# Kernel optimization log

Measured on AMD Instinct MI355X. Metric: run time of the kernel, lower is better.

Reference implementation:

```python
import jax, jax.numpy as jnp
import numpy as np
from itertools import combinations

WIRES, LAYERS, CUTOFF, OUT_WIRES, BATCH = 4, 2, 10, 3, 2048

def _annih(c):
    # annihilation operator a in the Fock basis, truncated to cutoff c
    return jnp.diag(jnp.sqrt(jnp.arange(1, c, dtype=jnp.float32)), 1).astype(jnp.complex64)

_expm = jnp.vectorize(jax.scipy.linalg.expm, signature='(n,n)->(n,n)')

def _squeeze(r, phi, a):
    # S(z) = exp((z* a^2 - z a+^2)/2), z = r e^{i phi}; r, phi have arbitrary batch shape
    z = (r * jnp.exp(1j * phi)).astype(jnp.complex64)[..., None, None]
    a2 = a @ a
    ad2 = a.conj().T @ a.conj().T
    return _expm(0.5 * (jnp.conj(z) * a2 - z * ad2))

def _disp(r, phi, a):
    # D(alpha) = exp(alpha a+ - alpha* a), alpha = r e^{i phi}
    al = (r * jnp.exp(1j * phi)).astype(jnp.complex64)[..., None, None]
    ad = a.conj().T
    return _expm(al * ad - jnp.conj(al) * a)

def _bs(theta, phi, a):
    # SF BSgate: B = exp(theta (e^{i phi} a b+ - e^{-i phi} a+ b))
    ad = a.conj().T
    G = theta * (jnp.exp(1j * phi) * jnp.kron(a, ad) - jnp.exp(-1j * phi) * jnp.kron(ad, a))
    return jax.scipy.linalg.expm(G.astype(jnp.complex64))

def _cx(s, a):
    # SF CXgate: exp(-i s x1 p2 / hbar) = exp(-(s/2) (a+a+) kron (b-b+)) with hbar=2
    ad = a.conj().T
    G = (-s / 2.0) * jnp.kron(a + ad, a - ad)
    return jax.scipy.linalg.expm(G.astype(jnp.complex64))

def _apply1(state, U, m):
    # apply single-mode gate U ([c,c] shared or [B,c,c] per-sample) to mode m
    if U.ndim == 2:
        return jnp.moveaxis(jnp.tensordot(state, U, axes=[[1 + m], [1]]), -1, 1 + m)
    st = jnp.moveaxis(state, 1 + m, -1)
    st = jnp.einsum('b...j,bij->b...i', st, U)
    return jnp.moveaxis(st, -1, 1 + m)

def _apply2(state, U4, m1, m2):
    # apply two-mode gate U4 [c,c,c,c] (out1,out2,in1,in2) to modes (m1, m2)
    st = jnp.moveaxis(state, (1 + m1, 1 + m2), (-2, -1))
    st = jnp.einsum('b...kl,ijkl->b...ij', st, U4)
    return jnp.moveaxis(st, (-2, -1), (1 + m1, 1 + m2))

def _forward(jets, s_scale, disp_mag, disp_phase, squeeze_mag, squeeze_phase, w_dense, b_dense):
    B, c = jets.shape[0], CUTOFF
    a = _annih(c)
    eta, phi, pt = jets[:, :, 0], jets[:, :, 1], jets[:, :, 2]  # each [B, WIRES]
    scale = 10.0 / (1.0 + jnp.exp(-s_scale)) + 0.01
    # vacuum |0...0> for every sample
    state = jnp.zeros((B,) + (c,) * WIRES, jnp.complex64)
    state = state.at[(slice(None),) + (0,) * WIRES].set(1.0)
    # per-sample data-encoding gates
    S_enc = _squeeze(eta, pt * phi / 2.0, a)      # [B, WIRES, c, c]
    D_enc = _disp(scale * pt, eta, a)             # [B, WIRES, c, c]
    for w in range(WIRES):
        state = _apply1(state, S_enc[:, w], w)
        state = _apply1(state, D_enc[:, w], w)
    # fixed entangling gates (shared across batch)
    CX = _cx(1.0, a).reshape(c, c, c, c)
    BS = _bs(jnp.pi / 4.0, jnp.pi / 2.0, a).reshape(c, c, c, c)
    # learned per-layer single-mode gates (shared across batch)
    S_lay = _squeeze(squeeze_mag, squeeze_phase, a)  # [LAYERS, WIRES, c, c]
    D_lay = _disp(disp_mag, disp_phase, a)
    for L in range(LAYERS):
        for (i, j) in combinations(range(WIRES), 2):
            state = _apply2(state, CX, i, j)
        for i in range(WIRES):
            state = _apply2(state, BS, i, (i + 1) % WIRES)
        for w in range(WIRES):
            state = _apply1(state, S_lay[L, w], w)
            state = _apply1(state, D_lay[L, w], w)
    probs = jnp.abs(state) ** 2
    nvec = jnp.arange(c, dtype=jnp.float32)
    photons = jnp.stack(
        [probs.sum(axis=tuple(1 + k for k in range(WIRES) if k != m)) @ nvec
         for m in range(OUT_WIRES)], axis=1)  # [B, OUT_WIRES] mean photon numbers
    return (photons @ w_dense + b_dense)[:, 0]  # [B]

def setup_inputs() -> dict:
    key = jax.random.key(0)
    ks = jax.random.split(key, 8)
    u = lambda k, sh: jax.random.uniform(k, sh, jnp.float32, -1.0, 1.0)
    return {
        'jets': 0.3 * jax.random.normal(ks[0], (BATCH, WIRES, 3), jnp.float32),
        's_scale': u(ks[1], ()),
        'disp_mag': u(ks[2], (LAYERS, WIRES)),
        'disp_phase': u(ks[3], (LAYERS, WIRES)),
        'squeeze_mag': u(ks[4], (LAYERS, WIRES)),
        'squeeze_phase': u(ks[5], (LAYERS, WIRES)),
        'w_dense': u(ks[6], (OUT_WIRES, 1)),
        'b_dense': jnp.zeros((1,), jnp.float32),
    }

def reference(jets, s_scale, disp_mag, disp_phase, squeeze_mag, squeeze_phase, w_dense, b_dense):
    return _forward(jets, s_scale, disp_mag, disp_phase, squeeze_mag, squeeze_phase, w_dense, b_dense)
```

## Files before the change

kernel.cpp:

```cpp
#include <hip/hip_runtime.h>
#include <math.h>


namespace {

constexpr int NTB = 1024;
constexpr int SMEM_STATE = 162352;
constexpr double THETA = 0.7853981633974483096;

struct cxf { float x, y; };
typedef float v2f __attribute__((ext_vector_type(2)));
typedef float v4f __attribute__((ext_vector_type(4)));

constexpr int U_OFF = 15872;

__device__ __forceinline__ cxf gen_squeeze_f(int i, int j, float zr, float zi){
  if (j == i+2){ float g = 0.5f*sqrtf((float)((i+1)*(i+2))); return {zr*g, -zi*g}; }
  if (i == j+2){ float g = 0.5f*sqrtf((float)((j+1)*(j+2))); return {-zr*g, -zi*g}; }
  return {0.f, 0.f};
}
__device__ __forceinline__ cxf gen_disp_f(int i, int j, float ar, float ai){
  if (i == j+1){ float g = sqrtf((float)i); return {ar*g, ai*g}; }
  if (j == i+1){ float g = sqrtf((float)j); return {-ar*g, ai*g}; }
  return {0.f, 0.f};
}

__device__ void expm_f32(bool act, int n, cxf* M, cxf* P, cxf* T, cxf* R, int lane){
  const int n2 = n*n;
  if (act){
    for (int e=lane; e<n2; e+=64){ M[e].x *= 0x1p-10f; M[e].y *= 0x1p-10f; }
    for (int e=lane; e<n2; e+=64){
      P[e] = M[e];
      cxf r = M[e];
      if (e % (n+1) == 0) r.x += 1.f;
      R[e] = r;
    }
  }
  __syncthreads();
  for (int t=2; t<=12; ++t){
    if (act){
      float inv = 1.f/(float)t;
      for (int e=lane; e<n2; e+=64){
        int i = e/n, j = e - i*n;
        float ax=0.f, ay=0.f;
        for (int k=0;k<n;k++){
          cxf p = P[i*n+k], m = M[k*n+j];
          ax += p.x*m.x - p.y*m.y;
          ay += p.x*m.y + p.y*m.x;
        }
        T[e] = {ax*inv, ay*inv};
      }
    }
    __syncthreads();
    { cxf* tmp = P; P = T; T = tmp; }
    if (act){ for (int e=lane; e<n2; e+=64){ R[e].x += P[e].x; R[e].y += P[e].y; } }
    __syncthreads();
  }
  for (int s=0; s<10; ++s){
    if (act){
      for (int e=lane; e<n2; e+=64){
        int i = e/n, j = e - i*n;
        float ax=0.f, ay=0.f;
        for (int k=0;k<n;k++){
          cxf p = R[i*n+k], q = R[k*n+j];
          ax += p.x*q.x - p.y*q.y;
          ay += p.x*q.y + p.y*q.x;
        }
        T[e] = {ax, ay};
      }
    }
    __syncthreads();
    { cxf* tmp = R; R = T; T = tmp; }
    __syncthreads();
  }
}

__global__ __launch_bounds__(256)
void gates_kernel(const float* __restrict__ dmag, const float* __restrict__ dphase,
                  const float* __restrict__ smag, const float* __restrict__ sphase,
                  float* __restrict__ wsf){
  __shared__ double lam[10];
  __shared__ float scr[4][4][200];
  const int tid = threadIdx.x;
  const int wv = tid >> 6, lane = tid & 63, g = blockIdx.x;
  float* ws_V  = wsf;
  float* ws_VT = wsf + 100;
  float* ws_W  = wsf + 200;
  cxf* ws_BS   = (cxf*)(wsf + 1200);
  cxf* ws_stage= (cxf*)(wsf + 6600);

  if (tid < 10){
    double lo = -6.0, hi = 6.0;
    for (int it=0; it<52; ++it){
      double mid = 0.5*(lo+hi);
      int cnt = 0;
      double pm1 = 1.0;
      double p = -mid;
      if (p == 0.0){ p = -1e-300; }
      if (p < 0.0) cnt++;
      for (int k=2; k<=10; ++k){
        double pn = -mid*p - (double)(k-1)*pm1;
        bool chg = (pn < 0.0) != (p < 0.0);
        if (pn == 0.0){ pn = (p < 0.0) ? 1e-300 : -1e-300; chg = true; }
        if (chg) cnt++;
        pm1 = p; p = pn;
      }
      if (cnt > tid) hi = mid; else lo = mid;
    }
    double x = 0.5*(lo+hi);
    double p[10];
    p[0] = 1.0; p[1] = x;
    for (int k=1;k<9;k++) p[k+1] = (x*p[k] - sqrt((double)k)*p[k-1]) * (1.0/sqrt((double)(k+1)));
    double nn=0.0; for (int k=0;k<10;k++) nn += p[k]*p[k];
    double inv = 1.0/sqrt(nn);
    lam[tid] = x;
    if (g == 0){
      for (int k=0;k<10;k++){
        float v = (float)(p[k]*inv);
        ws_V[k*10+tid]  = v;
        ws_VT[tid*10+k] = v;
      }
    }
  }
  __syncthreads();

  int t = g*4 + wv;
  bool act = (t < 45);
  int n = 10, bn = 0, ilo = 0;
  if (act && t >= 10 && t < 29){
    bn = t - 10; ilo = bn < 10 ? 0 : bn - 9;
    int ihi = bn < 10 ? bn : 9;
    n = ihi - ilo + 1;
  }
  cxf* M = (cxf*)scr[wv][0];
  cxf* P = (cxf*)scr[wv][1];
  cxf* T = (cxf*)scr[wv][2];
  cxf* R = (cxf*)scr[wv][3];
  if (act){
    if (t < 10){
      float l = (float)lam[t];
      for (int e=lane; e<100; e+=64){
        int i=e/10, j=e-10*i;
        float v = 0.f;
        if (j == i+1) v = -0.5f*l*sqrtf((float)(i+1));
        else if (i == j+1) v = 0.5f*l*sqrtf((float)i);
        M[e] = {v, 0.f};
      }
    } else if (t < 29){
      for (int e=lane; e<n*n; e+=64){
        int rr=e/n, c=e-n*rr;
        float v = 0.f;
        if (c == rr+1) v = (float)THETA*sqrtf((float)((ilo+rr+1)*(bn-ilo-rr)));
        else if (rr == c+1) v = (float)THETA*sqrtf((float)((ilo+c+1)*(bn-ilo-c)));
        M[e] = {0.f, v};
      }
    } else {
      int idx = t-29, kind = idx>>3, L=(idx>>2)&1, w=idx&3;
      float r_ = kind ? dmag[L*4+w]   : smag[L*4+w];
      float ph = kind ? dphase[L*4+w] : sphase[L*4+w];
      float zr = r_*cosf(ph), zi = r_*sinf(ph);
      for (int e=lane; e<100; e+=64){
        int i=e/10, j=e-10*i;
        M[e] = kind ? gen_disp_f(i,j,zr,zi) : gen_squeeze_f(i,j,zr,zi);
      }
    }
  }
  __syncthreads();
  expm_f32(act, n, M, P, T, R, lane);
  if (act){
    if (t < 10){
      for (int e=lane;e<100;e+=64){
        int i=e/10, j=e-10*i;
        ws_W[t*100 + j*10 + i] = R[e].x;
      }
    } else if (t < 29){
      for (int e=lane;e<100;e+=64){
        int rr=e/10, c=e-10*rr;
        cxf o; o.x=0.f; o.y=0.f;
        if (rr < n && c < n) o = R[rr*n+c];
        ws_BS[bn*100 + c*10 + rr] = o;
      }
    } else {
      int idx = t-29;
      for (int e=lane;e<100;e+=64) ws_stage[idx*100 + e] = R[e];
    }
  }
}

__global__ __launch_bounds__(512)
void fuse_kernel(float* __restrict__ wsf){
  __shared__ cxf ulraw[8][100];
  const int tid = threadIdx.x, wv = tid>>6, lane = tid&63;
  const cxf* stage = (const cxf*)(wsf + 6600);
  cxf* ws_UL = (cxf*)(wsf + 5000);
  cxf* ws_WU = (cxf*)(wsf + 9800);
  const float* V  = wsf;
  const float* Wt = wsf + 200;
  const cxf* Sm = stage + wv*100;
  const cxf* Dm = stage + (8+wv)*100;
  for (int e=lane; e<100; e+=64){
    int i=e/10, j=e-10*i;
    float ax=0.f, ay=0.f;
    for (int k=0;k<10;k++){
      cxf d=Dm[i*10+k], s=Sm[k*10+j];
      ax += d.x*s.x - d.y*s.y;
      ay += d.x*s.y + d.y*s.x;
    }
    ulraw[wv][e] = {ax, ay};
  }
  __syncthreads();
  cxf t0={0.f,0.f}, t1={0.f,0.f};
  if (wv == 0){
    {
      int e=lane, i=e/10, j=e-10*i;
      float ox=0.f, oy=0.f;
      for (int k=0;k<10;k++){ float v=V[k*10+i]; ox+=v*ulraw[0][k*10+j].x; oy+=v*ulraw[0][k*10+j].y; }
      t0 = {ox, oy};
    }
    if (lane+64 < 100){
      int e=lane+64, i=e/10, j=e-10*i;
      float ox=0.f, oy=0.f;
      for (int k=0;k<10;k++){ float v=V[k*10+i]; ox+=v*ulraw[0][k*10+j].x; oy+=v*ulraw[0][k*10+j].y; }
      t1 = {ox, oy};
    }
  }
  __syncthreads();
  if (wv == 0){
    ulraw[0][lane] = t0;
    if (lane+64 < 100) ulraw[0][lane+64] = t1;
  }
  __syncthreads();
  for (int e=tid; e<400; e+=512){
    int fi = e/100, r = e-100*fi;
    int f = (fi==0) ? 0 : (3+fi);
    int i=r/10, j=r-10*i;
    ws_UL[f*100 + j*10 + i] = ulraw[f][i*10+j];
  }
  for (int round=0; round<4; ++round){
    int id = round*8 + wv;
    if (id < 30){
      int b = 1 + id/10, n = id - (id/10)*10;
      const cxf* Ub = ulraw[b];
      for (int e=lane; e<100; e+=64){
        int i=e/10, j=e-10*i;
        float ax=0.f, ay=0.f;
        for (int k=0;k<10;k++){
          float w = Wt[n*100 + k*10 + i];
          ax += w*Ub[k*10+j].x;
          ay += w*Ub[k*10+j].y;
        }
        cxf o; o.x=ax; o.y=ay;
        ws_WU[id*100 + j*10 + i] = o;
      }
    }
  }
}

__global__ __launch_bounds__(128)
void enc_kernel(const float* __restrict__ jets, const float* __restrict__ sscale,
                float* __restrict__ wsf){
  __shared__ float scr[2][4][200];
  __shared__ cxf col[10];
  __shared__ cxf uacc[10];
  const int tid = threadIdx.x, wv = tid>>6, lane = tid&63;
  const int blk = blockIdx.x, b = blk>>2, w = blk&3;

  float eta = jets[b*12 + w*3 + 0];
  float jph = jets[b*12 + w*3 + 1];
  float pt  = jets[b*12 + w*3 + 2];

  cxf* M = (cxf*)scr[wv][0];
  cxf* P = (cxf*)scr[wv][1];
  cxf* T = (cxf*)scr[wv][2];
  cxf* R = (cxf*)scr[wv][3];
  {
    float zr, zi;
    if (wv == 0){ float phs = pt*jph*0.5f; zr = eta*cosf(phs); zi = eta*sinf(phs); }
    else {
      double sc = 10.0/(1.0 + exp(-(double)sscale[0])) + 0.01;
      float mag = (float)sc*pt; zr = mag*cosf(eta); zi = mag*sinf(eta);
    }
    for (int e=lane; e<100; e+=64){
      int i=e/10, j=e-10*i;
      M[e] = wv ? gen_disp_f(i,j,zr,zi) : gen_squeeze_f(i,j,zr,zi);
    }
  }
  __syncthreads();
  expm_f32(true, 10, M, P, T, R, lane);
  cxf* Rs = (cxf*)scr[0][3];
  cxf* Rd = (cxf*)scr[1][3];
  if (tid < 10) col[tid] = Rs[tid*10];
  __syncthreads();
  if (tid < 10){
    float ax=0.f, ay=0.f;
    for (int k=0;k<10;k++){
      cxf d = Rd[tid*10+k], c = col[k];
      ax += d.x*c.x - d.y*c.y;
      ay += d.x*c.y + d.y*c.x;
    }
    uacc[tid] = {ax, ay};
  }
  __syncthreads();
  if (tid < 10){
    float rx, ry;
    if (w == 0){
      rx = 0.f; ry = 0.f;
      for (int k=0;k<10;k++){
        float v = wsf[k*10 + tid];
        rx += v*uacc[k].x;
        ry += v*uacc[k].y;
      }
    } else { rx = uacc[tid].x; ry = uacc[tid].y; }
    float* u_out = wsf + U_OFF + (b*40 + w*10 + tid)*2;
    u_out[0] = rx;
    u_out[1] = ry;
  }
}

__device__ __forceinline__ constexpr int WS(int w){
  return w==0 ? 1010 : (w==1 ? 101 : (w==2 ? 10 : 1));
}

#define DECLP(P) v4f P##0={0.f,0.f,0.f,0.f}, P##1=P##0, P##2=P##0, P##3=P##0, \
  P##4=P##0, P##5=P##0, P##6=P##0, P##7=P##0, P##8=P##0, P##9=P##0;

#define REX(O,i,u) O##i = __builtin_elementwise_fma((v4f){(u),(u),(u),(u)}, vv, O##i);

#define RPAIRX(O, va, vb, Mp_) { \
  const v4f* Mp = (Mp_); \
  v4f q0=Mp[0],q1=Mp[1],q2=Mp[2],q3=Mp[3],q4=Mp[4]; \
  { v4f vv=va; REX(O,0,q0.x) REX(O,1,q0.y) REX(O,2,q0.z) REX(O,3,q0.w) REX(O,4,q1.x) \
               REX(O,5,q1.y) REX(O,6,q1.z) REX(O,7,q1.w) REX(O,8,q2.x) REX(O,9,q2.y) } \
  { v4f vv=vb; REX(O,0,q2.z) REX(O,1,q2.w) REX(O,2,q3.x) REX(O,3,q3.y) REX(O,4,q3.z) \
               REX(O,5,q3.w) REX(O,6,q4.x) REX(O,7,q4.y) REX(O,8,q4.z) REX(O,9,q4.w) } }

#define RSTAGE(Mt, I, O) \
  RPAIRX(O, I##0, I##1, (const v4f*)((Mt)+0))  \
  RPAIRX(O, I##2, I##3, (const v4f*)((Mt)+20)) \
  RPAIRX(O, I##4, I##5, (const v4f*)((Mt)+40)) \
  RPAIRX(O, I##6, I##7, (const v4f*)((Mt)+60)) \
  RPAIRX(O, I##8, I##9, (const v4f*)((Mt)+80))

#define CEX(O,i,ur,ui) \
  O##i = __builtin_elementwise_fma((v4f){(ur),(ur),(ur),(ur)}, vv, O##i); \
  O##i = __builtin_elementwise_fma((v4f){-(ui),(ui),-(ui),(ui)}, vs, O##i);

#define CROWX(O, vk, Up_) { \
  const v4f* Up = (Up_); \
  v4f q0=Up[0],q1=Up[1],q2=Up[2],q3=Up[3],q4=Up[4]; \
  v4f vv=vk, vs=__builtin_shufflevector(vk,vk,1,0,3,2); \
  CEX(O,0,q0.x,q0.y) CEX(O,1,q0.z,q0.w) CEX(O,2,q1.x,q1.y) CEX(O,3,q1.z,q1.w) \
  CEX(O,4,q2.x,q2.y) CEX(O,5,q2.z,q2.w) CEX(O,6,q3.x,q3.y) CEX(O,7,q3.z,q3.w) \
  CEX(O,8,q4.x,q4.y) CEX(O,9,q4.z,q4.w) }

#define CROWX9(O, vk, Up_) { \
  const v4f* Up = (Up_); \
  v4f q0=Up[0],q1=Up[1],q2=Up[2],q3=Up[3],q4=Up[4]; \
  v4f vv=vk, vs=__builtin_shufflevector(vk,vk,1,0,3,2); \
  CEX(O,1,q0.z,q0.w) CEX(O,2,q1.x,q1.y) CEX(O,3,q1.z,q1.w) \
  CEX(O,4,q2.x,q2.y) CEX(O,5,q2.z,q2.w) CEX(O,6,q3.x,q3.y) CEX(O,7,q3.z,q3.w) \
  CEX(O,8,q4.x,q4.y) CEX(O,9,q4.z,q4.w) }

#define CSTAGE(U, I, O) \
  CROWX(O, I##0, (const v4f*)((U)+0))  CROWX(O, I##1, (const v4f*)((U)+10)) \
  CROWX(O, I##2, (const v4f*)((U)+20)) CROWX(O, I##3, (const v4f*)((U)+30)) \
  CROWX(O, I##4, (const v4f*)((U)+40)) CROWX(O, I##5, (const v4f*)((U)+50)) \
  CROWX(O, I##6, (const v4f*)((U)+60)) CROWX(O, I##7, (const v4f*)((U)+70)) \
  CROWX(O, I##8, (const v4f*)((U)+80)) CROWX(O, I##9, (const v4f*)((U)+90))

#define CSTAGE9(U, I, O) \
  CROWX9(O, I##0, (const v4f*)((U)+0))  CROWX9(O, I##1, (const v4f*)((U)+10)) \
  CROWX9(O, I##2, (const v4f*)((U)+20)) CROWX9(O, I##3, (const v4f*)((U)+30)) \
  CROWX9(O, I##4, (const v4f*)((U)+40)) CROWX9(O, I##5, (const v4f*)((U)+50)) \
  CROWX9(O, I##6, (const v4f*)((U)+60)) CROWX9(O, I##7, (const v4f*)((U)+70)) \
  CROWX9(O, I##8, (const v4f*)((U)+80)) CROWX9(O, I##9, (const v4f*)((U)+90))

#define LDS_RD10 \
  v4f r0=S[base], r1=S[base+sm], r2=S[base+2*sm], r3=S[base+3*sm], r4=S[base+4*sm], \
      r5=S[base+5*sm], r6=S[base+6*sm], r7=S[base+7*sm], r8=S[base+8*sm], r9=S[base+9*sm];

#define PSTORE10(P) { S[base]=P##0; S[base+sm]=P##1; S[base+2*sm]=P##2; S[base+3*sm]=P##3; \
  S[base+4*sm]=P##4; S[base+5*sm]=P##5; S[base+6*sm]=P##6; S[base+7*sm]=P##7; \
  S[base+8*sm]=P##8; S[base+9*sm]=P##9; }

__device__ __forceinline__ void fuse_w1_r(v4f* S, const float* __restrict__ Wall,
                                          const float* __restrict__ Mu, int tid){
  if (tid < 1000){
    int d0=tid/100, rem=tid-100*d0, d1=rem/10, d2=rem-10*d1;
    const int sm = 101;
    int base = d0*1010 + d1*10 + d2;
    LDS_RD10
    const float* M1 = Wall + d0*100;
    DECLP(a) RSTAGE(M1, r, a)
    DECLP(b) RSTAGE(Mu, a, b)
    PSTORE10(b)
  }
}
__device__ __forceinline__ void fuse_w1_c(v4f* S, const cxf* __restrict__ WUb,
                                          const float* __restrict__ Mu, int tid){
  if (tid < 1000){
    int d0=tid/100, rem=tid-100*d0, d1=rem/10, d2=rem-10*d1;
    const int sm = 101;
    int base = d0*1010 + d1*10 + d2;
    LDS_RD10
    const cxf* U1 = WUb + d0*100;
    DECLP(a) CSTAGE(U1, r, a)
    DECLP(b) RSTAGE(Mu, a, b)
    PSTORE10(b)
  }
}
__device__ __forceinline__ void fuse_w2_r(v4f* S, const float* __restrict__ Wall,
                                          const float* __restrict__ Mu, int tid){
  if (tid < 1000){
    int d0=tid/100, rem=tid-100*d0, d1=rem/10, d2=rem-10*d1;
    const int sm = 10;
    int base = d0*1010 + d1*101 + d2;
    LDS_RD10
    const float* M1 = Wall + d0*100;
    const float* M2 = Wall + d1*100;
    DECLP(a) RSTAGE(M1, r, a)
    DECLP(b) RSTAGE(M2, a, b)
    DECLP(c) RSTAGE(Mu, b, c)
    PSTORE10(c)
  }
}
__device__ __forceinline__ void fuse_w2_c(v4f* S, const cxf* __restrict__ WUb,
                                          const float* __restrict__ Wall,
                                          const float* __restrict__ Mu, int tid){
  if (tid < 1000){
    int d0=tid/100, rem=tid-100*d0, d1=rem/10, d2=rem-10*d1;
    const int sm = 10;
    int base = d0*1010 + d1*101 + d2;
    LDS_RD10
    const cxf* U1 = WUb + d0*100;
    const float* M2 = Wall + d1*100;
    DECLP(a) CSTAGE(U1, r, a)
    DECLP(b) RSTAGE(M2, a, b)
    DECLP(c) RSTAGE(Mu, b, c)
    PSTORE10(c)
  }
}
__device__ __forceinline__ void fuse_w3_r(v4f* S, const float* __restrict__ Wall, int tid){
  if (tid < 1000){
    int d0=tid/100, rem=tid-100*d0, d1=rem/10, d2=rem-10*d1;
    const int sm = 1;
    int base = d0*1010 + d2*101 + d1*10;
    LDS_RD10
    const float* M1 = Wall + d0*100;
    const float* M2 = Wall + d2*100;
    const float* M3 = Wall + d1*100;
    DECLP(a) RSTAGE(M1, r, a)
    DECLP(b) RSTAGE(M2, a, b)
    DECLP(c) RSTAGE(M3, b, c)
    PSTORE10(c)
  }
}
__device__ __forceinline__ void fuse_w3_c(v4f* S, const cxf* __restrict__ WUb,
                                          const float* __restrict__ Wall, int tid){
  if (tid < 1000){
    int d0=tid/100, rem=tid-100*d0, d1=rem/10, d2=rem-10*d1;
    const int sm = 1;
    int base = d0*1010 + d2*101 + d1*10;
    LDS_RD10
    const cxf* U1 = WUb + d0*100;
    const float* M2 = Wall + d2*100;
    const float* M3 = Wall + d1*100;
    DECLP(a) CSTAGE(U1, r, a)
    DECLP(b) RSTAGE(M2, a, b)
    DECLP(c) RSTAGE(M3, b, c)
    PSTORE10(c)
  }
}

__device__ __forceinline__ void apply1_r4(v4f* S, const float* __restrict__ Mt, int m, int tid){
  const int sm = WS(m);
  const int x0 = (m==0)?1:0, x1=(m<=1)?2:1, x2=(m<=2)?3:2;
  const int s0 = WS(x0), s1 = WS(x1), s2 = WS(x2);
  if (tid < 1000){
    int d0=tid/100, rem=tid-100*d0, d1=rem/10, d2=rem-10*d1;
    int base = d0*s0 + d1*s1 + d2*s2;
    LDS_RD10
    DECLP(a) RSTAGE(Mt, r, a)
    PSTORE10(a)
  }
}

__device__ __forceinline__ void apply1_c4(v4f* S, const cxf* __restrict__ U, int m, int tid){
  const int sm = WS(m);
  const int x0 = (m==0)?1:0, x1=(m<=1)?2:1, x2=(m<=2)?3:2;
  const int s0 = WS(x0), s1 = WS(x1), s2 = WS(x2);
  if (tid < 1000){
    int d0=tid/100, rem=tid-100*d0, d1=rem/10, d2=rem-10*d1;
    int base = d0*s0 + d1*s1 + d2*s2;
    LDS_RD10
    DECLP(a) CSTAGE(U, r, a)
    PSTORE10(a)
  }
}

__device__ __forceinline__ v2f measure14(const v4f* S, const cxf* __restrict__ U, int m, int tid){
  const int sm = WS(m);
  const int x0 = (m==0)?1:0, x1=(m<=1)?2:1, x2=3;
  const int s0 = WS(x0), s1 = WS(x1), s2 = WS(x2);
  v2f s = {0.f, 0.f};
  if (tid < 1000){
    int d0=tid/100, rem=tid-100*d0, d1=rem/10, d2=rem-10*d1;
    int base = d0*s0 + d1*s1 + d2*s2;
    LDS_RD10
    DECLP(a) CSTAGE9(U, r, a)
    #define MQ4(i) { s.x += (float)(i)*(a##i.x*a##i.x + a##i.y*a##i.y); \
                     s.y += (float)(i)*(a##i.z*a##i.z + a##i.w*a##i.w); }
    MQ4(1) MQ4(2) MQ4(3) MQ4(4) MQ4(5) MQ4(6) MQ4(7) MQ4(8) MQ4(9)
    #undef MQ4
  }
  return s;
}

#define BSTQ(r) if ((r) < sz){ S[wadr] = a##r; wadr += ds; }
#define BSTQ_ALL BSTQ(0) BSTQ(1) BSTQ(2) BSTQ(3) BSTQ(4) BSTQ(5) BSTQ(6) BSTQ(7) BSTQ(8) BSTQ(9)
__device__ __forceinline__ void applyBS4(v4f* S, const cxf* __restrict__ BSp, int m1, int m2, int tid){
  int ra=-1, rb=-1;
  for (int q=0;q<4;q++) if (q!=m1 && q!=m2){ if (ra<0) ra=q; else rb=q; }
  const int sa0 = WS(ra), sb0 = WS(rb);
  const bool sw = (sa0==101 && sb0==10);
  const int sa = sw ? sb0 : sa0, sb = sw ? sa0 : sb0;
  const int s1 = WS(m1), s2 = WS(m2);
  const int ds = s1 - s2;
  #pragma unroll 1
  for (int w0=0; w0<2048; w0+=NTB){
    int it = w0 + tid;
    if (it < 1900){
      int bn = it/100, rest = it-100*bn;
      int ilo = bn<10?0:bn-9, ihi = bn<10?bn:9, sz = ihi-ilo+1;
      int ca = rest/10, cb = rest-10*ca;
      int base = ca*sa + cb*sb;
      const cxf* __restrict__ Bt = BSp + bn*100;
      DECLP(a)
      int radr = base + ilo*s1 + (bn-ilo)*s2;
      int kk = 0;
      #pragma unroll 1
      for (int c=0;c<sz;c++){
        v4f rk = S[radr];
        CROWX(a, rk, (const v4f*)(Bt + kk))
        radr += ds; kk += 10;
      }
      int wadr = base + ilo*s1 + (bn-ilo)*s2;
      BSTQ_ALL
    }
  }
}

__global__ __launch_bounds__(NTB)
__attribute__((amdgpu_waves_per_eu(4)))
void state_kernel(const float* __restrict__ wd, const float* __restrict__ bd,
                  const float* __restrict__ wsf, float* __restrict__ out){
  extern __shared__ __align__(16) char smem[];
  v4f* S    = (v4f*)smem;
  cxf* uv   = (cxf*)(smem + 161584);
  v2f* red  = (v2f*)(smem + 162224);

  const float* __restrict__ V   = wsf;
  const float* __restrict__ VT  = wsf + 100;
  const float* __restrict__ W   = wsf + 200;
  const cxf*   __restrict__ BSm = (const cxf*)(wsf + 1200);
  const cxf*   __restrict__ UL  = (const cxf*)(wsf + 5000);
  const cxf*   __restrict__ WU  = (const cxf*)(wsf + 9800);
  const cxf*   __restrict__ uw  = (const cxf*)(wsf + U_OFF);

  const int tid = threadIdx.x, wv = tid>>6, lane = tid&63;
  const int b = blockIdx.x;

  if (tid < 80) uv[tid] = uw[b*80 + tid];
  __syncthreads();

  for (int e=tid; e<10000; e+=NTB){
    int c0=e/1000, r_=e-1000*c0, c1=r_/100, r2_=r_-100*c1, c2=r2_/10, c3=r2_-10*c2;
    cxf A0 = uv[c0],    B0 = uv[10+c1], C0 = uv[20+c2], D0 = uv[30+c3];
    cxf A1 = uv[40+c0], B1 = uv[50+c1], C1 = uv[60+c2], D1 = uv[70+c3];
    float pr = A0.x*B0.x - A0.y*B0.y, pi = A0.x*B0.y + A0.y*B0.x;
    float qr = pr*C0.x - pi*C0.y,  qi = pr*C0.y + pi*C0.x;
    float e0r = qr*D0.x - qi*D0.y, e0i = qr*D0.y + qi*D0.x;
    pr = A1.x*B1.x - A1.y*B1.y; pi = A1.x*B1.y + A1.y*B1.x;
    qr = pr*C1.x - pi*C1.y;  qi = pr*C1.y + pi*C1.x;
    float e1r = qr*D1.x - qi*D1.y, e1i = qr*D1.y + qi*D1.x;
    S[c0*1010 + c1*101 + c2*10 + c3] = (v4f){e0r, e0i, e1r, e1i};
  }
  __syncthreads();

  fuse_w1_r(S, W, V, tid);   __syncthreads();
  fuse_w2_r(S, W, V, tid);   __syncthreads();
  fuse_w3_r(S, W, tid);      __syncthreads();
  apply1_r4(S, VT, 0, tid);  __syncthreads();
  apply1_r4(S, VT, 1, tid);  __syncthreads();
  apply1_r4(S, VT, 2, tid);  __syncthreads();
  applyBS4(S, BSm, 0, 1, tid); __syncthreads();
  applyBS4(S, BSm, 1, 2, tid); __syncthreads();
  applyBS4(S, BSm, 2, 3, tid); __syncthreads();
  applyBS4(S, BSm, 3, 0, tid); __syncthreads();
  apply1_c4(S, UL, 0, tid);  __syncthreads();

  fuse_w1_c(S, WU,        V, tid); __syncthreads();
  fuse_w2_c(S, WU + 1000, W, V, tid); __syncthreads();
  fuse_w3_c(S, WU + 2000, W, tid); __syncthreads();
  apply1_r4(S, VT, 0, tid);  __syncthreads();
  apply1_r4(S, VT, 1, tid);  __syncthreads();
  apply1_r4(S, VT, 2, tid);  __syncthreads();
  applyBS4(S, BSm, 0, 1, tid); __syncthreads();
  applyBS4(S, BSm, 1, 2, tid); __syncthreads();
  applyBS4(S, BSm, 2, 3, tid); __syncthreads();
  applyBS4(S, BSm, 3, 0, tid); __syncthreads();

  float w0 = wd[0], w1 = wd[1], w2 = wd[2];
  v2f m0 = measure14(S, UL + 400, 0, tid);
  v2f m1 = measure14(S, UL + 500, 1, tid);
  v2f m2 = measure14(S, UL + 600, 2, tid);
  v2f acc;
  acc.x = w0*m0.x + w1*m1.x + w2*m2.x;
  acc.y = w0*m0.y + w1*m1.y + w2*m2.y;

  for (int off=32; off; off>>=1){
    acc.x += __shfl_down(acc.x, off, 64);
    acc.y += __shfl_down(acc.y, off, 64);
  }
  if (lane == 0) red[wv] = acc;
  __syncthreads();
  if (tid == 0){
    float sx = 0.f, sy = 0.f;
    for (int i=0;i<16;i++){ sx += red[i].x; sy += red[i].y; }
    out[2*b+0] = sx + bd[0];
    out[2*b+1] = sy + bd[0];
  }
}

}

extern "C" void kernel_launch(void* const* d_in, const int* in_sizes, int n_in,
                              void* d_out, int out_size, void* d_ws, size_t ws_size,
                              hipStream_t stream){
  const float* jets   = (const float*)d_in[0];
  const float* sscale = (const float*)d_in[1];
  const float* dmag   = (const float*)d_in[2];
  const float* dphase = (const float*)d_in[3];
  const float* smag   = (const float*)d_in[4];
  const float* sphase = (const float*)d_in[5];
  const float* wd     = (const float*)d_in[6];
  const float* bd     = (const float*)d_in[7];
  float* out = (float*)d_out;
  float* wsf = (float*)d_ws;
  int B = in_sizes[0] / 12;

  (void)hipFuncSetAttribute(reinterpret_cast<const void*>(&state_kernel),
                            hipFuncAttributeMaxDynamicSharedMemorySize, SMEM_STATE);

  gates_kernel<<<12, 256, 0, stream>>>(dmag, dphase, smag, sphase, wsf);
  fuse_kernel<<<1, 512, 0, stream>>>(wsf);
  enc_kernel<<<B*4, 128, 0, stream>>>(jets, sscale, wsf);
  state_kernel<<<B/2, NTB, SMEM_STATE, stream>>>(wd, bd, wsf, out);
}
```

Measured before the change: 821.5 us.

## Assign wave-uniform matrix tasks to reduce divergent per-thread matrix loads

```diff
diff --git a/kernel.cpp b/kernel.cpp
--- a/kernel.cpp
+++ b/kernel.cpp
@@ -383,93 +383,80 @@
   S[base+4*sm]=P##4; S[base+5*sm]=P##5; S[base+6*sm]=P##6; S[base+7*sm]=P##7; \
   S[base+8*sm]=P##8; S[base+9*sm]=P##9; }
 
-__device__ __forceinline__ void fuse_w1_r(v4f* S, const float* __restrict__ Wall,
-                                          const float* __restrict__ Mu, int tid){
-  if (tid < 1000){
-    int d0=tid/100, rem=tid-100*d0, d1=rem/10, d2=rem-10*d1;
-    const int sm = 101;
-    int base = d0*1010 + d1*10 + d2;
+__device__ __forceinline__ void do_Wtask(v4f* S, const float* __restrict__ Wall,
+                                         int sc, int sm, int sa, int sb,
+                                         int t, int lane){
+  int n = t>>1, half = t&1;
+  if (lane < 50){
+    int f = half*50 + lane;
+    int qa = f/10, qb = f - 10*qa;
+    int base = n*sc + qa*sa + qb*sb;
+    const float* __restrict__ Mt = Wall + n*100;
     LDS_RD10
-    const float* M1 = Wall + d0*100;
-    DECLP(a) RSTAGE(M1, r, a)
-    DECLP(b) RSTAGE(Mu, a, b)
-    PSTORE10(b)
-  }
-}
-__device__ __forceinline__ void fuse_w1_c(v4f* S, const cxf* __restrict__ WUb,
-                                          const float* __restrict__ Mu, int tid){
-  if (tid < 1000){
-    int d0=tid/100, rem=tid-100*d0, d1=rem/10, d2=rem-10*d1;
-    const int sm = 101;
-    int base = d0*1010 + d1*10 + d2;
+    DECLP(a) RSTAGE(Mt, r, a)
+    PSTORE10(a)
+  }
+}
+__device__ __forceinline__ void applyW_u(v4f* S, const float* __restrict__ Wall,
+                                         int sc, int sm, int sa, int sb,
+                                         int wid, int lane){
+  do_Wtask(S, Wall, sc, sm, sa, sb, wid, lane);
+  if (wid < 4) do_Wtask(S, Wall, sc, sm, sa, sb, 16+wid, lane);
+}
+
+__device__ __forceinline__ void do_WUtask(v4f* S, const cxf* __restrict__ WUb,
+                                          int sc, int sm, int sa, int sb,
+                                          int t, int lane){
+  int n = t>>1, half = t&1;
+  if (lane < 50){
+    int f = half*50 + lane;
+    int qa = f/10, qb = f - 10*qa;
+    int base = n*sc + qa*sa + qb*sb;
+    const cxf* __restrict__ U = WUb + n*100;
     LDS_RD10
-    const cxf* U1 = WUb + d0*100;
-    DECLP(a) CSTAGE(U1, r, a)
-    DECLP(b) RSTAGE(Mu, a, b)
-    PSTORE10(b)
-  }
-}
-__device__ __forceinline__ void fuse_w2_r(v4f* S, const float* __restrict__ Wall,
-                                          const float* __restrict__ Mu, int tid){
-  if (tid < 1000){
-    int d0=tid/100, rem=tid-100*d0, d1=rem/10, d2=rem-10*d1;
-    const int sm = 10;
-    int base = d0*1010 + d1*101 + d2;
-    LDS_RD10
-    const float* M1 = Wall + d0*100;
-    const float* M2 = Wall + d1*100;
-    DECLP(a) RSTAGE(M1, r, a)
-    DECLP(b) RSTAGE(M2, a, b)
-    DECLP(c) RSTAGE(Mu, b, c)
-    PSTORE10(c)
-  }
-}
-__device__ __forceinline__ void fuse_w2_c(v4f* S, const cxf* __restrict__ WUb,
-                                          const float* __restrict__ Wall,
-                                          const float* __restrict__ Mu, int tid){
-  if (tid < 1000){
-    int d0=tid/100, rem=tid-100*d0, d1=rem/10, d2=rem-10*d1;
-    const int sm = 10;
-    int base = d0*1010 + d1*101 + d2;
-    LDS_RD10
-    const cxf* U1 = WUb + d0*100;
-    const float* M2 = Wall + d1*100;
-    DECLP(a) CSTAGE(U1, r, a)
-    DECLP(b) RSTAGE(M2, a, b)
-    DECLP(c) RSTAGE(Mu, b, c)
-    PSTORE10(c)
-  }
-}
-__device__ __forceinline__ void fuse_w3_r(v4f* S, const float* __restrict__ Wall, int tid){
-  if (tid < 1000){
-    int d0=tid/100, rem=tid-100*d0, d1=rem/10, d2=rem-10*d1;
-    const int sm = 1;
-    int base = d0*1010 + d2*101 + d1*10;
-    LDS_RD10
-    const float* M1 = Wall + d0*100;
-    const float* M2 = Wall + d2*100;
-    const float* M3 = Wall + d1*100;
-    DECLP(a) RSTAGE(M1, r, a)
-    DECLP(b) RSTAGE(M2, a, b)
-    DECLP(c) RSTAGE(M3, b, c)
-    PSTORE10(c)
-  }
-}
-__device__ __forceinline__ void fuse_w3_c(v4f* S, const cxf* __restrict__ WUb,
-                                          const float* __restrict__ Wall, int tid){
-  if (tid < 1000){
-    int d0=tid/100, rem=tid-100*d0, d1=rem/10, d2=rem-10*d1;
-    const int sm = 1;
-    int base = d0*1010 + d2*101 + d1*10;
-    LDS_RD10
-    const cxf* U1 = WUb + d0*100;
-    const float* M2 = Wall + d2*100;
-    const float* M3 = Wall + d1*100;
-    DECLP(a) CSTAGE(U1, r, a)
-    DECLP(b) RSTAGE(M2, a, b)
-    DECLP(c) RSTAGE(M3, b, c)
-    PSTORE10(c)
-  }
+    DECLP(a) CSTAGE(U, r, a)
+    PSTORE10(a)
+  }
+}
+__device__ __forceinline__ void applyWU_u(v4f* S, const cxf* __restrict__ WUb,
+                                          int sc, int sm, int sa, int sb,
+                                          int wid, int lane){
+  do_WUtask(S, WUb, sc, sm, sa, sb, wid, lane);
+  if (wid < 4) do_WUtask(S, WUb, sc, sm, sa, sb, 16+wid, lane);
+}
+
+__device__ __forceinline__ void do_BStask(v4f* S, const cxf* __restrict__ BSp,
+                                          int sa, int sb, int s1, int s2, int ds,
+                                          int t, int lane){
+  int bn = t>>1, half = t&1;
+  int ilo = bn<10?0:bn-9, ihi = bn<10?bn:9, sz = ihi-ilo+1;
+  if (lane < 50){
+    int f = half*50 + lane;
+    int ca = f/10, cb = f - 10*ca;
+    int base = ca*sa + cb*sb;
+    const cxf* __restrict__ Bt = BSp + bn*100;
+    DECLP(a)
+    int radr = base + ilo*s1 + (bn-ilo)*s2;
+    int kk = 0;
+    #pragma unroll 1
+    for (int c=0;c<sz;c++){
+      v4f rk = S[radr];
+      CROWX(a, rk, (const v4f*)(Bt + kk))
+      radr += ds; kk += 10;
+    }
+    int wadr = base + ilo*s1 + (bn-ilo)*s2;
+    #define BSTQ(r) if ((r) < sz){ S[wadr] = a##r; wadr += ds; }
+    BSTQ(0) BSTQ(1) BSTQ(2) BSTQ(3) BSTQ(4) BSTQ(5) BSTQ(6) BSTQ(7) BSTQ(8) BSTQ(9)
+    #undef BSTQ
+  }
+}
+__device__ __forceinline__ void applyBS_u(v4f* S, const cxf* __restrict__ BSp,
+                                          int sa, int sb, int s1, int s2,
+                                          int wid, int lane){
+  const int ds = s1 - s2;
+  do_BStask(S, BSp, sa, sb, s1, s2, ds, wid, lane);
+  do_BStask(S, BSp, sa, sb, s1, s2, ds, wid+16, lane);
+  if (wid < 6) do_BStask(S, BSp, sa, sb, s1, s2, ds, wid+32, lane);
 }
 
 __device__ __forceinline__ void apply1_r4(v4f* S, const float* __restrict__ Mt, int m, int tid){
@@ -516,40 +503,6 @@
   return s;
 }
 
-#define BSTQ(r) if ((r) < sz){ S[wadr] = a##r; wadr += ds; }
-#define BSTQ_ALL BSTQ(0) BSTQ(1) BSTQ(2) BSTQ(3) BSTQ(4) BSTQ(5) BSTQ(6) BSTQ(7) BSTQ(8) BSTQ(9)
-__device__ __forceinline__ void applyBS4(v4f* S, const cxf* __restrict__ BSp, int m1, int m2, int tid){
-  int ra=-1, rb=-1;
-  for (int q=0;q<4;q++) if (q!=m1 && q!=m2){ if (ra<0) ra=q; else rb=q; }
-  const int sa0 = WS(ra), sb0 = WS(rb);
-  const bool sw = (sa0==101 && sb0==10);
-  const int sa = sw ? sb0 : sa0, sb = sw ? sa0 : sb0;
-  const int s1 = WS(m1), s2 = WS(m2);
-  const int ds = s1 - s2;
-  #pragma unroll 1
-  for (int w0=0; w0<2048; w0+=NTB){
-    int it = w0 + tid;
-    if (it < 1900){
-      int bn = it/100, rest = it-100*bn;
-      int ilo = bn<10?0:bn-9, ihi = bn<10?bn:9, sz = ihi-ilo+1;
-      int ca = rest/10, cb = rest-10*ca;
-      int base = ca*sa + cb*sb;
-      const cxf* __restrict__ Bt = BSp + bn*100;
-      DECLP(a)
-      int radr = base + ilo*s1 + (bn-ilo)*s2;
-      int kk = 0;
-      #pragma unroll 1
-      for (int c=0;c<sz;c++){
-        v4f rk = S[radr];
-        CROWX(a, rk, (const v4f*)(Bt + kk))
-        radr += ds; kk += 10;
-      }
-      int wadr = base + ilo*s1 + (bn-ilo)*s2;
-      BSTQ_ALL
-    }
-  }
-}
-
 __global__ __launch_bounds__(NTB)
 __attribute__((amdgpu_waves_per_eu(4)))
 void state_kernel(const float* __restrict__ wd, const float* __restrict__ bd,
@@ -568,6 +521,7 @@
   const cxf*   __restrict__ uw  = (const cxf*)(wsf + U_OFF);
 
   const int tid = threadIdx.x, wv = tid>>6, lane = tid&63;
+  const int wid = __builtin_amdgcn_readfirstlane(tid) >> 6;
   const int b = blockIdx.x;
 
   if (tid < 80) uv[tid] = uw[b*80 + tid];
@@ -587,28 +541,38 @@
   }
   __syncthreads();
 
-  fuse_w1_r(S, W, V, tid);   __syncthreads();
-  fuse_w2_r(S, W, V, tid);   __syncthreads();
-  fuse_w3_r(S, W, tid);      __syncthreads();
-  apply1_r4(S, VT, 0, tid);  __syncthreads();
-  apply1_r4(S, VT, 1, tid);  __syncthreads();
-  apply1_r4(S, VT, 2, tid);  __syncthreads();
-  applyBS4(S, BSm, 0, 1, tid); __syncthreads();
-  applyBS4(S, BSm, 1, 2, tid); __syncthreads();
-  applyBS4(S, BSm, 2, 3, tid); __syncthreads();
-  applyBS4(S, BSm, 3, 0, tid); __syncthreads();
-  apply1_c4(S, UL, 0, tid);  __syncthreads();
-
-  fuse_w1_c(S, WU,        V, tid); __syncthreads();
-  fuse_w2_c(S, WU + 1000, W, V, tid); __syncthreads();
-  fuse_w3_c(S, WU + 2000, W, tid); __syncthreads();
-  apply1_r4(S, VT, 0, tid);  __syncthreads();
-  apply1_r4(S, VT, 1, tid);  __syncthreads();
-  apply1_r4(S, VT, 2, tid);  __syncthreads();
-  applyBS4(S, BSm, 0, 1, tid); __syncthreads();
-  applyBS4(S, BSm, 1, 2, tid); __syncthreads();
-  applyBS4(S, BSm, 2, 3, tid); __syncthreads();
-  applyBS4(S, BSm, 3, 0, tid); __syncthreads();
+  applyW_u(S, W, 1010, 101, 10, 1, wid, lane); __syncthreads();
+  applyW_u(S, W, 1010, 10, 101, 1, wid, lane); __syncthreads();
+  applyW_u(S, W, 1010, 1, 10, 101, wid, lane); __syncthreads();
+  apply1_r4(S, VT, 0, tid); __syncthreads();
+  apply1_r4(S, V, 1, tid);  __syncthreads();
+  applyW_u(S, W, 101, 10, 1010, 1, wid, lane); __syncthreads();
+  applyW_u(S, W, 101, 1, 1010, 10, wid, lane); __syncthreads();
+  apply1_r4(S, VT, 1, tid); __syncthreads();
+  apply1_r4(S, V, 2, tid);  __syncthreads();
+  applyW_u(S, W, 10, 1, 1010, 101, wid, lane); __syncthreads();
+  apply1_r4(S, VT, 2, tid); __syncthreads();
+  applyBS_u(S, BSm, 10, 1, 1010, 101, wid, lane); __syncthreads();
+  applyBS_u(S, BSm, 1010, 1, 101, 10, wid, lane); __syncthreads();
+  applyBS_u(S, BSm, 1010, 101, 10, 1, wid, lane); __syncthreads();
+  applyBS_u(S, BSm, 10, 101, 1, 1010, wid, lane); __syncthreads();
+  apply1_c4(S, UL, 0, tid); __syncthreads();
+
+  applyWU_u(S, WU,        1010, 101, 10, 1, wid, lane); __syncthreads();
+  applyWU_u(S, WU + 1000, 1010, 10, 101, 1, wid, lane); __syncthreads();
+  applyWU_u(S, WU + 2000, 1010, 1, 10, 101, wid, lane); __syncthreads();
+  apply1_r4(S, VT, 0, tid); __syncthreads();
+  apply1_r4(S, V, 1, tid);  __syncthreads();
+  applyW_u(S, W, 101, 10, 1010, 1, wid, lane); __syncthreads();
+  applyW_u(S, W, 101, 1, 1010, 10, wid, lane); __syncthreads();
+  apply1_r4(S, VT, 1, tid); __syncthreads();
+  apply1_r4(S, V, 2, tid);  __syncthreads();
+  applyW_u(S, W, 10, 1, 1010, 101, wid, lane); __syncthreads();
+  apply1_r4(S, VT, 2, tid); __syncthreads();
+  applyBS_u(S, BSm, 10, 1, 1010, 101, wid, lane); __syncthreads();
+  applyBS_u(S, BSm, 1010, 1, 101, 10, wid, lane); __syncthreads();
+  applyBS_u(S, BSm, 1010, 101, 10, 1, wid, lane); __syncthreads();
+  applyBS_u(S, BSm, 10, 101, 1, 1010, wid, lane); __syncthreads();
 
   float w0 = wd[0], w1 = wd[1], w2 = wd[2];
   v2f m0 = measure14(S, UL + 400, 0, tid);
```

Measured after the change: 768.5 us. -6.4%, faster.
